# Optimization experiments

Measured on AMD Instinct MI355X. Metric: run time of the kernel, lower is better.

## Reference

```python
import jax, jax.numpy as jnp
import numpy as np

NUM_HEADS = 4
SPLIT = 2
DIM_FULL = 384  # constructor dim; scale uses dim // num_heads
SCALE = (DIM_FULL // NUM_HEADS) ** -0.5


def img2windows(img, ws, nh):
    # img: (B, D, H, W, C) -> (num_windows, nh, N, C//nh), N = prod(ws)
    B, D, H, W, C = img.shape
    d, h, w = ws
    x = img.reshape(B, D // d, d, H // h, h, W // w, w, C)
    x = x.transpose(0, 1, 3, 5, 2, 4, 6, 7).reshape(-1, d * h * w, C)
    return x.reshape(-1, d * h * w, nh, C // nh).transpose(0, 2, 1, 3)


def windows2img(xw, ws, B, D, H, W):
    # xw: (num_windows, d, h, w, C) -> (B, D, H, W, C)
    d, h, w = ws
    x = xw.reshape(B, D // d, H // h, W // w, d, h, w, -1)
    return x.transpose(0, 1, 4, 2, 5, 3, 6, 7).reshape(B, D, H, W, -1)


def setup_inputs() -> dict:
    key = jax.random.key(0)
    ks = jax.random.split(key, 5)
    B, D, H, W, C = 2, 8, 64, 64, 96
    qkv = jax.random.normal(ks[0], (3, B, D, H, W, C), jnp.float32)
    conv_w = jax.random.normal(ks[1], (C, 1, 3, 3, 3), jnp.float32) * 0.1  # depthwise Conv3d weight (O, I/groups, kD, kH, kW)
    conv_b = jax.random.normal(ks[2], (C,), jnp.float32) * 0.01
    proj_w = jax.random.normal(ks[3], (C, C), jnp.float32) * (C ** -0.5)  # torch Linear weight (out, in)
    proj_b = jax.random.normal(ks[4], (C,), jnp.float32) * 0.01
    return {"qkv": qkv, "conv_w": conv_w, "conv_b": conv_b, "proj_w": proj_w, "proj_b": proj_b}


def reference(qkv, conv_w, conv_b, proj_w, proj_b):
    q, k, v = qkv[0], qkv[1], qkv[2]
    B, D, H, W, C = q.shape
    ws = (1, H, SPLIT)  # idx == 0: (D_sp, H_sp, W_sp) = (1, H, split_size)
    qw = img2windows(q, ws, NUM_HEADS) * SCALE  # (nw, nh, N, hd)
    kw = img2windows(k, ws, NUM_HEADS)
    vw = img2windows(v, ws, NUM_HEADS)
    # LePE: depthwise 3x3x3 conv over v in NCDHW layout
    x = v.transpose(0, 4, 1, 2, 3)
    lepe = jax.lax.conv_general_dilated(
        x, conv_w, window_strides=(1, 1, 1), padding=[(1, 1)] * 3,
        dimension_numbers=("NCDHW", "OIDHW", "NCDHW"),
        feature_group_count=C) + conv_b[None, :, None, None, None]
    lepe = lepe.transpose(0, 2, 3, 4, 1)
    lepew = img2windows(lepe, ws, NUM_HEADS)
    # per-window attention
    attn = jax.nn.softmax(jnp.einsum("whnd,whmd->whnm", qw, kw), axis=-1)
    out = jnp.einsum("whnm,whmd->whnd", attn, vw) + lepew  # (nw, nh, N, hd)
    N = qw.shape[2]
    out = out.transpose(0, 2, 1, 3).reshape(-1, N, C)
    out = out @ proj_w.T + proj_b
    out = out.reshape(-1, ws[0], ws[1], ws[2], C)
    return windows2img(out, ws, B, D, H, W)
```

## Files before the change

### kernel.cpp

```cpp
#include <hip/hip_runtime.h>
#include <hip/hip_bf16.h>

constexpr int D_ = 8, H_ = 64, W_ = 64, C_ = 96;
constexpr int WC    = W_ * C_;
constexpr int HWC   = H_ * W_ * C_;
constexpr int BDHWC = 2 * D_ * HWC;
constexpr float SCALE = 0.10206207261596577f;

typedef __attribute__((ext_vector_type(4))) float f32x4;
typedef __attribute__((ext_vector_type(8))) short s16x8;

__device__ inline ushort f2bf(float x) {
  union { __hip_bfloat16 h; ushort u; } c;
  c.h = __float2bfloat16(x);
  return c.u;
}
__device__ inline float bf2f(ushort u) {
  union { float f; unsigned i; } c;
  c.i = ((unsigned)u) << 16;
  return c.f;
}
__device__ inline int xswz8(int bid, int nwg) {
  return (bid & 7) * (nwg >> 3) + (bid >> 3);
}

constexpr int QSTR  = 40;
constexpr int PSTR  = 136;
constexpr int PSTR2 = 72;

template <bool WSOUT>
__global__ void __launch_bounds__(256, 4)
attn_mfma_kernel(const float* __restrict__ qkv, float* __restrict__ out,
                 ushort* __restrict__ ws) {
  __shared__ ushort sK[128 * QSTR];
  __shared__ ushort sVt[32 * PSTR];
  __shared__ ushort sP[128 * PSTR2];

  const int t    = threadIdx.x;
  const int bid  = xswz8(blockIdx.x, 2048);
  const int head = bid & 3;
  const int nw   = bid >> 2;
  const int wq   = nw & 31;
  const int d    = (nw >> 5) & 7;
  const int b    = nw >> 8;
  const int hc   = head * 24;

  const float* qpl = qkv + (size_t)(b * 8 + d) * HWC;
  const float* kpl = qpl + BDHWC;
  const float* vpl = kpl + BDHWC;
  ushort* wvpl = ws + BDHWC + (size_t)(b * 8 + d) * HWC;

  {
    const s16x8 Z = {0, 0, 0, 0, 0, 0, 0, 0};
    int row = t >> 1, col = 24 + (t & 1) * 8;
    *reinterpret_cast<s16x8*>(&sK[row * QSTR + col]) = Z;
    if (t < 136) *reinterpret_cast<s16x8*>(&sVt[24 * PSTR + t * 8]) = Z;
  }

  #pragma unroll
  for (int it = 0; it < 3; ++it) {
    int idx = t + it * 256;
    int tok = idx / 6, c4 = (idx - tok * 6) * 4;
    int g = (tok >> 1) * WC + (wq * 2 + (tok & 1)) * 96 + hc + c4;
    float4 kv = *reinterpret_cast<const float4*>(kpl + g);
    float4 vv = *reinterpret_cast<const float4*>(vpl + g);
    ushort4 kh = { f2bf(kv.x), f2bf(kv.y), f2bf(kv.z), f2bf(kv.w) };
    ushort4 vh = { f2bf(vv.x), f2bf(vv.y), f2bf(vv.z), f2bf(vv.w) };
    *reinterpret_cast<ushort4*>(&sK[tok * QSTR + c4]) = kh;
    sVt[(c4 + 0) * PSTR + tok] = vh.x;
    sVt[(c4 + 1) * PSTR + tok] = vh.y;
    sVt[(c4 + 2) * PSTR + tok] = vh.z;
    sVt[(c4 + 3) * PSTR + tok] = vh.w;
    if (WSOUT) *reinterpret_cast<ushort4*>(wvpl + g) = vh;
  }

  const int wv = t >> 6, lane = t & 63;
  const int lr = lane & 15;
  const int lg = lane >> 4;
  const int r0 = (2 * wv) * 16;
  const int r1 = (2 * wv + 1) * 16;

  s16x8 a0 = {0,0,0,0,0,0,0,0}, a1 = {0,0,0,0,0,0,0,0};
  if (lg < 3) {
    union { s16x8 v; ushort u[8]; } qa;
    int tok = r0 + lr;
    const float* qp = qpl + (tok >> 1) * WC + (wq * 2 + (tok & 1)) * 96 + hc + lg * 8;
    float4 x0 = *reinterpret_cast<const float4*>(qp);
    float4 x1 = *reinterpret_cast<const float4*>(qp + 4);
    qa.u[0] = f2bf(x0.x * SCALE); qa.u[1] = f2bf(x0.y * SCALE);
    qa.u[2] = f2bf(x0.z * SCALE); qa.u[3] = f2bf(x0.w * SCALE);
    qa.u[4] = f2bf(x1.x * SCALE); qa.u[5] = f2bf(x1.y * SCALE);
    qa.u[6] = f2bf(x1.z * SCALE); qa.u[7] = f2bf(x1.w * SCALE);
    a0 = qa.v;
    tok = r1 + lr;
    qp = qpl + (tok >> 1) * WC + (wq * 2 + (tok & 1)) * 96 + hc + lg * 8;
    x0 = *reinterpret_cast<const float4*>(qp);
    x1 = *reinterpret_cast<const float4*>(qp + 4);
    qa.u[0] = f2bf(x0.x * SCALE); qa.u[1] = f2bf(x0.y * SCALE);
    qa.u[2] = f2bf(x0.z * SCALE); qa.u[3] = f2bf(x0.w * SCALE);
    qa.u[4] = f2bf(x1.x * SCALE); qa.u[5] = f2bf(x1.y * SCALE);
    qa.u[6] = f2bf(x1.z * SCALE); qa.u[7] = f2bf(x1.w * SCALE);
    a1 = qa.v;
  }

  __syncthreads();

  float rsum[2][4];
  #pragma unroll
  for (int rb = 0; rb < 2; ++rb)
    #pragma unroll
    for (int r = 0; r < 4; ++r) rsum[rb][r] = 0.f;

  f32x4 accO[2][2];
  #pragma unroll
  for (int i = 0; i < 2; ++i)
    #pragma unroll
    for (int j = 0; j < 2; ++j) accO[i][j] = f32x4{0.f, 0.f, 0.f, 0.f};

  #pragma unroll
  for (int half = 0; half < 2; ++half) {
    f32x4 accS[2][4];
    #pragma unroll
    for (int i = 0; i < 2; ++i)
      #pragma unroll
      for (int j = 0; j < 4; ++j) accS[i][j] = f32x4{0.f, 0.f, 0.f, 0.f};

    #pragma unroll
    for (int nb = 0; nb < 4; ++nb) {
      s16x8 bb = *reinterpret_cast<const s16x8*>(
          &sK[(half * 64 + nb * 16 + lr) * QSTR + lg * 8]);
      accS[0][nb] = __builtin_amdgcn_mfma_f32_16x16x32_bf16(a0, bb, accS[0][nb], 0, 0, 0);
      accS[1][nb] = __builtin_amdgcn_mfma_f32_16x16x32_bf16(a1, bb, accS[1][nb], 0, 0, 0);
    }

    #pragma unroll
    for (int rb = 0; rb < 2; ++rb)
      #pragma unroll
      for (int nb = 0; nb < 4; ++nb)
        #pragma unroll
        for (int r = 0; r < 4; ++r) {
          float e = __expf(accS[rb][nb][r]);
          accS[rb][nb][r] = e;
          rsum[rb][r] += e;
        }

    if (half) __syncthreads();

    #pragma unroll
    for (int rb = 0; rb < 2; ++rb)
      #pragma unroll
      for (int nb = 0; nb < 4; ++nb)
        #pragma unroll
        for (int r = 0; r < 4; ++r)
          sP[((2 * wv + rb) * 16 + lg * 4 + r) * PSTR2 + nb * 16 + lr] =
              f2bf(accS[rb][nb][r]);
    __syncthreads();

    #pragma unroll
    for (int kb = 0; kb < 2; ++kb) {
      int kc = half * 64 + kb * 32 + lg * 8;
      s16x8 pa0 = *reinterpret_cast<const s16x8*>(&sP[(r0 + lr) * PSTR2 + kb * 32 + lg * 8]);
      s16x8 pa1 = *reinterpret_cast<const s16x8*>(&sP[(r1 + lr) * PSTR2 + kb * 32 + lg * 8]);
      s16x8 vb0 = *reinterpret_cast<const s16x8*>(&sVt[lr * PSTR + kc]);
      s16x8 vb1 = *reinterpret_cast<const s16x8*>(&sVt[(16 + lr) * PSTR + kc]);
      accO[0][0] = __builtin_amdgcn_mfma_f32_16x16x32_bf16(pa0, vb0, accO[0][0], 0, 0, 0);
      accO[0][1] = __builtin_amdgcn_mfma_f32_16x16x32_bf16(pa0, vb1, accO[0][1], 0, 0, 0);
      accO[1][0] = __builtin_amdgcn_mfma_f32_16x16x32_bf16(pa1, vb0, accO[1][0], 0, 0, 0);
      accO[1][1] = __builtin_amdgcn_mfma_f32_16x16x32_bf16(pa1, vb1, accO[1][1], 0, 0, 0);
    }
  }

  float* opl   = out + (size_t)(b * 8 + d) * HWC;
  ushort* wpl  = ws  + (size_t)(b * 8 + d) * HWC;
  #pragma unroll
  for (int rb = 0; rb < 2; ++rb) {
    #pragma unroll
    for (int r = 0; r < 4; ++r) {
      float s = rsum[rb][r];
      s += __shfl_xor(s, 1); s += __shfl_xor(s, 2);
      s += __shfl_xor(s, 4); s += __shfl_xor(s, 8);
      int tok = (2 * wv + rb) * 16 + lg * 4 + r;
      int g = (tok >> 1) * WC + (wq * 2 + (tok & 1)) * 96 + hc;
      float inv = 1.0f / s;
      if (WSOUT) {
        wpl[g + lr] = f2bf(accO[rb][0][r] * inv);
        if (lr < 8) wpl[g + 16 + lr] = f2bf(accO[rb][1][r] * inv);
      } else {
        opl[g + lr] = accO[rb][0][r] * inv;
        if (lr < 8) opl[g + 16 + lr] = accO[rb][1][r] * inv;
      }
    }
  }
}

constexpr int VSTR = 104;
constexpr int WSTR = 104;

template <bool WSIN>
__global__ void __launch_bounds__(256, 4)
lepe_proj_fused_kernel(const float* __restrict__ qkv, const float* __restrict__ cw,
                       const float* __restrict__ cbias, const float* __restrict__ pw,
                       const float* __restrict__ pb, float* __restrict__ io,
                       const ushort* __restrict__ ws) {
  __shared__ ushort sV[66 * VSTR];
  __shared__ ushort sW[96 * WSTR];
  __shared__ ushort sCW[27 * 96];
  __shared__ float  sCB[96];
  __shared__ float  sPB[96];

  const int t   = threadIdx.x;
  const int bid = xswz8(blockIdx.x, 1024);
  const int h   = bid & 63;
  const int d   = (bid >> 6) & 7;
  const int b   = bid >> 9;

  float* iop = io + (size_t)(b * 8 + d) * HWC + h * WC;
  const ushort* wsp = ws + (size_t)(b * 8 + d) * HWC + h * WC;
  const ushort* wvb = ws + BDHWC + (size_t)b * 8 * HWC;
  const float* vbatch = qkv + 2 * (size_t)BDHWC + (size_t)b * 8 * HWC;

  const int tt  = t >> 2;
  const int cbk = (t & 3) * 24;

  float lep[24];
  if (WSIN) {
    union { s16x8 v; ushort u[8]; } azu[3];
    #pragma unroll
    for (int k = 0; k < 3; ++k)
      azu[k].v = *reinterpret_cast<const s16x8*>(wsp + tt * 96 + cbk + k * 8);
    #pragma unroll
    for (int k = 0; k < 3; ++k)
      #pragma unroll
      for (int e = 0; e < 8; ++e) lep[8*k+e] = bf2f(azu[k].u[e]);
  } else {
    float4 az[6];
    #pragma unroll
    for (int j = 0; j < 6; ++j)
      az[j] = *reinterpret_cast<const float4*>(iop + tt * 96 + cbk + j * 4);
    #pragma unroll
    for (int j = 0; j < 6; ++j) {
      lep[4*j+0] = az[j].x; lep[4*j+1] = az[j].y;
      lep[4*j+2] = az[j].z; lep[4*j+3] = az[j].w;
    }
  }

  if (t < 26) {
    const s16x8 Z = {0, 0, 0, 0, 0, 0, 0, 0};
    int row = (t < 13) ? 0 : 65;
    int col = (t < 13 ? t : t - 13) * 8;
    *reinterpret_cast<s16x8*>(&sV[row * VSTR + col]) = Z;
  }

  #pragma unroll
  for (int it = 0; it < 9; ++it) {
    int idx = t + it * 256;
    int co = idx / 24, c4 = (idx - co * 24) * 4;
    float4 x = *reinterpret_cast<const float4*>(pw + co * 96 + c4);
    ushort4 hx = { f2bf(x.x), f2bf(x.y), f2bf(x.z), f2bf(x.w) };
    *reinterpret_cast<ushort4*>(&sW[co * WSTR + c4]) = hx;
  }
  for (int idx = t; idx < 2592; idx += 256) {
    int c = idx / 27, tap = idx - c * 27;
    sCW[tap * 96 + c] = f2bf(cw[idx]);
  }
  if (t < 96) { sCB[t] = cbias[t]; sPB[t] = pb[t]; }

  #define TAP(row, tap)                                                      \
    {                                                                        \
      _Pragma("unroll")                                                      \
      for (int j8 = 0; j8 < 3; ++j8) {                                       \
        union { s16x8 v; ushort u[8]; } vu;                                  \
        vu.v = *reinterpret_cast<const s16x8*>(&sV[(row) * VSTR + cbk + j8 * 8]); \
        union { s16x8 v; ushort u[8]; } wu;                                  \
        wu.v = *reinterpret_cast<const s16x8*>(&sCW[(tap) * 96 + cbk + j8 * 8]); \
        _Pragma("unroll")                                                    \
        for (int e = 0; e < 8; ++e)                                          \
          lep[8*j8+e] = fmaf(bf2f(vu.u[e]), bf2f(wu.u[e]), lep[8*j8+e]);     \
      }                                                                      \
    }

  #pragma unroll
  for (int dd = 0; dd < 3; ++dd) {
    int zd = d + dd - 1;
    if (zd < 0 || zd >= D_) continue;
    #pragma unroll
    for (int dh = 0; dh < 3; ++dh) {
      int zh = h + dh - 1;
      if (zh < 0 || zh >= H_) continue;
      __syncthreads();
      if (WSIN) {
        const ushort* vrow = wvb + (size_t)zd * HWC + zh * WC;
        #pragma unroll
        for (int it = 0; it < 3; ++it) {
          int idx = t + it * 256;
          int tok = idx / 12, c8 = idx - tok * 12;
          s16x8 x = *reinterpret_cast<const s16x8*>(vrow + tok * 96 + c8 * 8);
          *reinterpret_cast<s16x8*>(&sV[(tok + 1) * VSTR + c8 * 8]) = x;
        }
      } else {
        const float4* src = reinterpret_cast<const float4*>(
            vbatch + (size_t)zd * HWC + zh * WC);
        #pragma unroll
        for (int it = 0; it < 6; ++it) {
          int idx = t + it * 256;
          int tok = idx / 24, c4 = idx - tok * 24;
          float4 x = src[idx];
          ushort4 hx = { f2bf(x.x), f2bf(x.y), f2bf(x.z), f2bf(x.w) };
          *reinterpret_cast<ushort4*>(&sV[(tok + 1) * VSTR + c4 * 4]) = hx;
        }
      }
      __syncthreads();
      const int tap0 = dd * 9 + dh * 3;
      TAP(tt,     tap0 + 0);
      TAP(tt + 1, tap0 + 1);
      TAP(tt + 2, tap0 + 2);
    }
  }
  #undef TAP

  __syncthreads();
  #pragma unroll
  for (int j = 0; j < 6; ++j) {
    float4 bz = *reinterpret_cast<const float4*>(sCB + cbk + j * 4);
    ushort4 hx = { f2bf(lep[4*j+0] + bz.x), f2bf(lep[4*j+1] + bz.y),
                   f2bf(lep[4*j+2] + bz.z), f2bf(lep[4*j+3] + bz.w) };
    *reinterpret_cast<ushort4*>(&sV[tt * VSTR + cbk + j * 4]) = hx;
  }
  __syncthreads();

  const int wv = t >> 6, lane = t & 63;
  const int lr = lane & 15, lg = lane >> 4;

  f32x4 acc[6];
  #pragma unroll
  for (int cb = 0; cb < 6; ++cb) {
    float bv = sPB[cb * 16 + lr];
    acc[cb] = f32x4{bv, bv, bv, bv};
  }
  s16x8 afr[3];
  #pragma unroll
  for (int kb = 0; kb < 3; ++kb)
    afr[kb] = *reinterpret_cast<const s16x8*>(&sV[(wv * 16 + lr) * VSTR + kb * 32 + lg * 8]);
  #pragma unroll
  for (int kb = 0; kb < 3; ++kb) {
    #pragma unroll
    for (int cb = 0; cb < 6; ++cb) {
      s16x8 bfr = *reinterpret_cast<const s16x8*>(&sW[(cb * 16 + lr) * WSTR + kb * 32 + lg * 8]);
      acc[cb] = __builtin_amdgcn_mfma_f32_16x16x32_bf16(afr[kb], bfr, acc[cb], 0, 0, 0);
    }
  }

  #pragma unroll
  for (int cb = 0; cb < 6; ++cb) {
    #pragma unroll
    for (int r = 0; r < 4; ++r) {
      int tok = wv * 16 + lg * 4 + r;
      iop[tok * 96 + cb * 16 + lr] = acc[cb][r];
    }
  }
}

extern "C" void kernel_launch(void* const* d_in, const int* in_sizes, int n_in,
                              void* d_out, int out_size, void* d_ws, size_t ws_size,
                              hipStream_t stream) {
  const float* qkv = (const float*)d_in[0];
  const float* cw  = (const float*)d_in[1];
  const float* cb  = (const float*)d_in[2];
  const float* pw  = (const float*)d_in[3];
  const float* pb  = (const float*)d_in[4];
  float* out = (float*)d_out;
  ushort* ws = (ushort*)d_ws;

  const size_t need = (size_t)2 * BDHWC * sizeof(ushort);
  if (ws_size >= need) {
    hipLaunchKernelGGL((attn_mfma_kernel<true>), dim3(2048), dim3(256), 0, stream,
                       qkv, out, ws);
    hipLaunchKernelGGL((lepe_proj_fused_kernel<true>), dim3(1024), dim3(256), 0, stream,
                       qkv, cw, cb, pw, pb, out, ws);
  } else {
    hipLaunchKernelGGL((attn_mfma_kernel<false>), dim3(2048), dim3(256), 0, stream,
                       qkv, out, ws);
    hipLaunchKernelGGL((lepe_proj_fused_kernel<false>), dim3(1024), dim3(256), 0, stream,
                       qkv, cw, cb, pw, pb, out, ws);
  }
}
```

Measured before the change: 56.66 us.

## Stage three H-rows of V per depth slice to cut barriers in LePE conv

The depthwise conv loop now loads all three neighbouring H rows for a given depth offset into three separate shared-memory buffers, with one barrier pair per depth slice instead of per (depth, height) pair. Out-of-range rows are zero-filled so the tap loop runs unconditionally. This cuts barriers and lets the row loads overlap, but it triples the sV footprint and lowers the launch-bounds occupancy hint from 4 to 2 blocks.

```diff
diff --git a/kernel.cpp b/kernel.cpp
--- a/kernel.cpp
+++ b/kernel.cpp
@@ -197,12 +197,12 @@
 constexpr int WSTR = 104;
 
 template <bool WSIN>
-__global__ void __launch_bounds__(256, 4)
+__global__ void __launch_bounds__(256, 2)
 lepe_proj_fused_kernel(const float* __restrict__ qkv, const float* __restrict__ cw,
                        const float* __restrict__ cbias, const float* __restrict__ pw,
                        const float* __restrict__ pb, float* __restrict__ io,
                        const ushort* __restrict__ ws) {
-  __shared__ ushort sV[66 * VSTR];
+  __shared__ ushort sV[3][66 * VSTR];
   __shared__ ushort sW[96 * WSTR];
   __shared__ ushort sCW[27 * 96];
   __shared__ float  sCB[96];
@@ -244,11 +244,12 @@
     }
   }
 
-  if (t < 26) {
+  if (t < 78) {
     const s16x8 Z = {0, 0, 0, 0, 0, 0, 0, 0};
-    int row = (t < 13) ? 0 : 65;
-    int col = (t < 13 ? t : t - 13) * 8;
-    *reinterpret_cast<s16x8*>(&sV[row * VSTR + col]) = Z;
+    int buf = t / 26, rr = t - buf * 26;
+    int row = (rr < 13) ? 0 : 65;
+    int col = (rr < 13 ? rr : rr - 13) * 8;
+    *reinterpret_cast<s16x8*>(&sV[buf][row * VSTR + col]) = Z;
   }
 
   #pragma unroll
@@ -265,12 +266,12 @@
   }
   if (t < 96) { sCB[t] = cbias[t]; sPB[t] = pb[t]; }
 
-  #define TAP(row, tap)                                                      \
+  #define TAP(BUF, row, tap)                                                 \
     {                                                                        \
       _Pragma("unroll")                                                      \
       for (int j8 = 0; j8 < 3; ++j8) {                                       \
         union { s16x8 v; ushort u[8]; } vu;                                  \
-        vu.v = *reinterpret_cast<const s16x8*>(&sV[(row) * VSTR + cbk + j8 * 8]); \
+        vu.v = *reinterpret_cast<const s16x8*>(&sV[BUF][(row) * VSTR + cbk + j8 * 8]); \
         union { s16x8 v; ushort u[8]; } wu;                                  \
         wu.v = *reinterpret_cast<const s16x8*>(&sCW[(tap) * 96 + cbk + j8 * 8]); \
         _Pragma("unroll")                                                    \
@@ -283,37 +284,51 @@
   for (int dd = 0; dd < 3; ++dd) {
     int zd = d + dd - 1;
     if (zd < 0 || zd >= D_) continue;
+    __syncthreads();
+
     #pragma unroll
     for (int dh = 0; dh < 3; ++dh) {
       int zh = h + dh - 1;
-      if (zh < 0 || zh >= H_) continue;
-      __syncthreads();
-      if (WSIN) {
-        const ushort* vrow = wvb + (size_t)zd * HWC + zh * WC;
+      if (zh >= 0 && zh < H_) {
+        if (WSIN) {
+          const ushort* vrow = wvb + (size_t)zd * HWC + zh * WC;
+          #pragma unroll
+          for (int it = 0; it < 3; ++it) {
+            int idx = t + it * 256;
+            int tok = idx / 12, c8 = idx - tok * 12;
+            s16x8 x = *reinterpret_cast<const s16x8*>(vrow + tok * 96 + c8 * 8);
+            *reinterpret_cast<s16x8*>(&sV[dh][(tok + 1) * VSTR + c8 * 8]) = x;
+          }
+        } else {
+          const float4* src = reinterpret_cast<const float4*>(
+              vbatch + (size_t)zd * HWC + zh * WC);
+          #pragma unroll
+          for (int it = 0; it < 6; ++it) {
+            int idx = t + it * 256;
+            int tok = idx / 24, c4 = idx - tok * 24;
+            float4 x = src[idx];
+            ushort4 hx = { f2bf(x.x), f2bf(x.y), f2bf(x.z), f2bf(x.w) };
+            *reinterpret_cast<ushort4*>(&sV[dh][(tok + 1) * VSTR + c4 * 4]) = hx;
+          }
+        }
+      } else {
+        const s16x8 Z = {0, 0, 0, 0, 0, 0, 0, 0};
         #pragma unroll
         for (int it = 0; it < 3; ++it) {
           int idx = t + it * 256;
           int tok = idx / 12, c8 = idx - tok * 12;
-          s16x8 x = *reinterpret_cast<const s16x8*>(vrow + tok * 96 + c8 * 8);
-          *reinterpret_cast<s16x8*>(&sV[(tok + 1) * VSTR + c8 * 8]) = x;
-        }
-      } else {
-        const float4* src = reinterpret_cast<const float4*>(
-            vbatch + (size_t)zd * HWC + zh * WC);
-        #pragma unroll
-        for (int it = 0; it < 6; ++it) {
-          int idx = t + it * 256;
-          int tok = idx / 24, c4 = idx - tok * 24;
-          float4 x = src[idx];
-          ushort4 hx = { f2bf(x.x), f2bf(x.y), f2bf(x.z), f2bf(x.w) };
-          *reinterpret_cast<ushort4*>(&sV[(tok + 1) * VSTR + c4 * 4]) = hx;
+          *reinterpret_cast<s16x8*>(&sV[dh][(tok + 1) * VSTR + c8 * 8]) = Z;
         }
       }
-      __syncthreads();
-      const int tap0 = dd * 9 + dh * 3;
-      TAP(tt,     tap0 + 0);
-      TAP(tt + 1, tap0 + 1);
-      TAP(tt + 2, tap0 + 2);
+    }
+    __syncthreads();
+
+    const int tap0 = dd * 9;
+    #pragma unroll
+    for (int dh = 0; dh < 3; ++dh) {
+      TAP(dh, tt,     tap0 + dh * 3 + 0);
+      TAP(dh, tt + 1, tap0 + dh * 3 + 1);
+      TAP(dh, tt + 2, tap0 + dh * 3 + 2);
     }
   }
   #undef TAP
@@ -324,7 +339,7 @@
     float4 bz = *reinterpret_cast<const float4*>(sCB + cbk + j * 4);
     ushort4 hx = { f2bf(lep[4*j+0] + bz.x), f2bf(lep[4*j+1] + bz.y),
                    f2bf(lep[4*j+2] + bz.z), f2bf(lep[4*j+3] + bz.w) };
-    *reinterpret_cast<ushort4*>(&sV[tt * VSTR + cbk + j * 4]) = hx;
+    *reinterpret_cast<ushort4*>(&sV[0][tt * VSTR + cbk + j * 4]) = hx;
   }
   __syncthreads();
 
@@ -340,7 +355,7 @@
   s16x8 afr[3];
   #pragma unroll
   for (int kb = 0; kb < 3; ++kb)
-    afr[kb] = *reinterpret_cast<const s16x8*>(&sV[(wv * 16 + lr) * VSTR + kb * 32 + lg * 8]);
+    afr[kb] = *reinterpret_cast<const s16x8*>(&sV[0][(wv * 16 + lr) * VSTR + kb * 32 + lg * 8]);
   #pragma unroll
   for (int kb = 0; kb < 3; ++kb) {
     #pragma unroll
```

Result: slower. 62.11 us (+9.6%).

## Double-buffer LePE row loads with async global-to-LDS DMA in fused proj kernel

Applied to the files above, without the earlier changes.

Reworks the depthwise-conv row staging in the fused LePE+projection kernel to use two LDS buffers filled by global_load_lds, so the next (d,h) row is prefetched while the current one is convolved. This cuts the sync/load latency between taps. Padded halo rows are replaced by clamped indices and multiplicative edge masks, and out-of-range rows are still loaded but skipped, which keeps control flow uniform. Launch bounds drop from 4 to 2 waves per EU to fit the larger LDS footprint, which may reduce occupancy.

```diff
diff --git a/kernel.cpp b/kernel.cpp
--- a/kernel.cpp
+++ b/kernel.cpp
@@ -193,16 +193,15 @@
   }
 }
 
-constexpr int VSTR = 104;
 constexpr int WSTR = 104;
 
 template <bool WSIN>
-__global__ void __launch_bounds__(256, 4)
+__global__ void __launch_bounds__(256, 2)
 lepe_proj_fused_kernel(const float* __restrict__ qkv, const float* __restrict__ cw,
                        const float* __restrict__ cbias, const float* __restrict__ pw,
                        const float* __restrict__ pb, float* __restrict__ io,
                        const ushort* __restrict__ ws) {
-  __shared__ ushort sV[66 * VSTR];
+  __shared__ ushort sV2[2][64 * 96];
   __shared__ ushort sW[96 * WSTR];
   __shared__ ushort sCW[27 * 96];
   __shared__ float  sCB[96];
@@ -214,6 +213,8 @@
   const int d   = (bid >> 6) & 7;
   const int b   = bid >> 9;
 
+  const int wvq = t >> 6, lane = t & 63;
+
   float* iop = io + (size_t)(b * 8 + d) * HWC + h * WC;
   const ushort* wsp = ws + (size_t)(b * 8 + d) * HWC + h * WC;
   const ushort* wvb = ws + BDHWC + (size_t)b * 8 * HWC;
@@ -242,13 +243,6 @@
       lep[4*j+0] = az[j].x; lep[4*j+1] = az[j].y;
       lep[4*j+2] = az[j].z; lep[4*j+3] = az[j].w;
     }
-  }
-
-  if (t < 26) {
-    const s16x8 Z = {0, 0, 0, 0, 0, 0, 0, 0};
-    int row = (t < 13) ? 0 : 65;
-    int col = (t < 13 ? t : t - 13) * 8;
-    *reinterpret_cast<s16x8*>(&sV[row * VSTR + col]) = Z;
   }
 
   #pragma unroll
@@ -265,12 +259,28 @@
   }
   if (t < 96) { sCB[t] = cbias[t]; sPB[t] = pb[t]; }
 
-  #define TAP(row, tap)                                                      \
+  int   zdc[3], zhc[3];
+  float fdc[3], fhc[3];
+  #pragma unroll
+  for (int j = 0; j < 3; ++j) {
+    int zd = d + j - 1;
+    fdc[j] = (zd >= 0 && zd < D_) ? 1.f : 0.f;
+    zdc[j] = zd < 0 ? 0 : (zd > D_ - 1 ? D_ - 1 : zd);
+    int zh = h + j - 1;
+    fhc[j] = (zh >= 0 && zh < H_) ? 1.f : 0.f;
+    zhc[j] = zh < 0 ? 0 : (zh > H_ - 1 ? H_ - 1 : zh);
+  }
+  const float fwl0 = (tt > 0)  ? 1.f : 0.f;
+  const float fwl2 = (tt < 63) ? 1.f : 0.f;
+  const int   zw0  = (tt > 0)  ? tt - 1 : 0;
+  const int   zw2  = (tt < 63) ? tt + 1 : 63;
+
+  #define TAPC(BI, row, tap)                                                 \
     {                                                                        \
       _Pragma("unroll")                                                      \
       for (int j8 = 0; j8 < 3; ++j8) {                                       \
         union { s16x8 v; ushort u[8]; } vu;                                  \
-        vu.v = *reinterpret_cast<const s16x8*>(&sV[(row) * VSTR + cbk + j8 * 8]); \
+        vu.v = *reinterpret_cast<const s16x8*>(&sV2[BI][(row) * 96 + cbk + j8 * 8]); \
         union { s16x8 v; ushort u[8]; } wu;                                  \
         wu.v = *reinterpret_cast<const s16x8*>(&sCW[(tap) * 96 + cbk + j8 * 8]); \
         _Pragma("unroll")                                                    \
@@ -278,26 +288,59 @@
           lep[8*j8+e] = fmaf(bf2f(vu.u[e]), bf2f(wu.u[e]), lep[8*j8+e]);     \
       }                                                                      \
     }
-
-  #pragma unroll
-  for (int dd = 0; dd < 3; ++dd) {
-    int zd = d + dd - 1;
-    if (zd < 0 || zd >= D_) continue;
-    #pragma unroll
-    for (int dh = 0; dh < 3; ++dh) {
-      int zh = h + dh - 1;
-      if (zh < 0 || zh >= H_) continue;
+  #define TAPE(BI, row, tap, FW)                                             \
+    {                                                                        \
+      _Pragma("unroll")                                                      \
+      for (int j8 = 0; j8 < 3; ++j8) {                                       \
+        union { s16x8 v; ushort u[8]; } vu;                                  \
+        vu.v = *reinterpret_cast<const s16x8*>(&sV2[BI][(row) * 96 + cbk + j8 * 8]); \
+        union { s16x8 v; ushort u[8]; } wu;                                  \
+        wu.v = *reinterpret_cast<const s16x8*>(&sCW[(tap) * 96 + cbk + j8 * 8]); \
+        _Pragma("unroll")                                                    \
+        for (int e = 0; e < 8; ++e)                                          \
+          lep[8*j8+e] = fmaf(bf2f(vu.u[e]) * (FW), bf2f(wu.u[e]), lep[8*j8+e]); \
+      }                                                                      \
+    }
+  #define DMA(zd, zh, BI)                                                    \
+    {                                                                        \
+      const ushort* vrow_ = wvb + (size_t)(zd) * HWC + (zh) * WC;            \
+      _Pragma("unroll")                                                      \
+      for (int c_ = 0; c_ < 3; ++c_) {                                       \
+        int ch_ = c_ * 4 + wvq;                                              \
+        __builtin_amdgcn_global_load_lds(                                    \
+            (const __attribute__((address_space(1))) void*)(vrow_ + ch_ * 512 + lane * 8), \
+            (__attribute__((address_space(3))) void*)(&sV2[BI][ch_ * 512]),  \
+            16, 0, 0);                                                       \
+      }                                                                      \
+    }
+
+  if (WSIN) {
+    DMA(zdc[0], zhc[0], 0);
+    __syncthreads();
+    #pragma unroll
+    for (int r = 0; r < 9; ++r) {
+      const int dd = r / 3, dh = r - 3 * dd;
+      if (r < 8) {
+        const int nr = r + 1, nd = nr / 3, nh = nr - 3 * nd;
+        DMA(zdc[nd], zhc[nh], nr & 1);
+      }
+      if (fdc[dd] * fhc[dh] != 0.f) {
+        TAPE(r & 1, zw0, r * 3 + 0, fwl0);
+        TAPC(r & 1, tt,  r * 3 + 1);
+        TAPE(r & 1, zw2, r * 3 + 2, fwl2);
+      }
       __syncthreads();
-      if (WSIN) {
-        const ushort* vrow = wvb + (size_t)zd * HWC + zh * WC;
-        #pragma unroll
-        for (int it = 0; it < 3; ++it) {
-          int idx = t + it * 256;
-          int tok = idx / 12, c8 = idx - tok * 12;
-          s16x8 x = *reinterpret_cast<const s16x8*>(vrow + tok * 96 + c8 * 8);
-          *reinterpret_cast<s16x8*>(&sV[(tok + 1) * VSTR + c8 * 8]) = x;
-        }
-      } else {
+    }
+  } else {
+    #pragma unroll
+    for (int dd = 0; dd < 3; ++dd) {
+      int zd = d + dd - 1;
+      if (zd < 0 || zd >= D_) continue;
+      #pragma unroll
+      for (int dh = 0; dh < 3; ++dh) {
+        int zh = h + dh - 1;
+        if (zh < 0 || zh >= H_) continue;
+        __syncthreads();
         const float4* src = reinterpret_cast<const float4*>(
             vbatch + (size_t)zd * HWC + zh * WC);
         #pragma unroll
@@ -306,29 +349,30 @@
           int tok = idx / 24, c4 = idx - tok * 24;
           float4 x = src[idx];
           ushort4 hx = { f2bf(x.x), f2bf(x.y), f2bf(x.z), f2bf(x.w) };
-          *reinterpret_cast<ushort4*>(&sV[(tok + 1) * VSTR + c4 * 4]) = hx;
+          *reinterpret_cast<ushort4*>(&sV2[0][tok * 96 + c4 * 4]) = hx;
         }
+        __syncthreads();
+        const int tap0 = dd * 9 + dh * 3;
+        TAPE(0, zw0, tap0 + 0, fwl0);
+        TAPC(0, tt,  tap0 + 1);
+        TAPE(0, zw2, tap0 + 2, fwl2);
       }
-      __syncthreads();
-      const int tap0 = dd * 9 + dh * 3;
-      TAP(tt,     tap0 + 0);
-      TAP(tt + 1, tap0 + 1);
-      TAP(tt + 2, tap0 + 2);
-    }
-  }
-  #undef TAP
-
-  __syncthreads();
+    }
+    __syncthreads();
+  }
+  #undef TAPC
+  #undef TAPE
+  #undef DMA
+
   #pragma unroll
   for (int j = 0; j < 6; ++j) {
     float4 bz = *reinterpret_cast<const float4*>(sCB + cbk + j * 4);
     ushort4 hx = { f2bf(lep[4*j+0] + bz.x), f2bf(lep[4*j+1] + bz.y),
                    f2bf(lep[4*j+2] + bz.z), f2bf(lep[4*j+3] + bz.w) };
-    *reinterpret_cast<ushort4*>(&sV[tt * VSTR + cbk + j * 4]) = hx;
+    *reinterpret_cast<ushort4*>(&sV2[0][tt * 96 + cbk + j * 4]) = hx;
   }
   __syncthreads();
 
-  const int wv = t >> 6, lane = t & 63;
   const int lr = lane & 15, lg = lane >> 4;
 
   f32x4 acc[6];
@@ -340,7 +384,7 @@
   s16x8 afr[3];
   #pragma unroll
   for (int kb = 0; kb < 3; ++kb)
-    afr[kb] = *reinterpret_cast<const s16x8*>(&sV[(wv * 16 + lr) * VSTR + kb * 32 + lg * 8]);
+    afr[kb] = *reinterpret_cast<const s16x8*>(&sV2[0][(wvq * 16 + lr) * 96 + kb * 32 + lg * 8]);
   #pragma unroll
   for (int kb = 0; kb < 3; ++kb) {
     #pragma unroll
@@ -354,7 +398,7 @@
   for (int cb = 0; cb < 6; ++cb) {
     #pragma unroll
     for (int r = 0; r < 4; ++r) {
-      int tok = wv * 16 + lg * 4 + r;
+      int tok = wvq * 16 + lg * 4 + r;
       iop[tok * 96 + cb * 16 + lr] = acc[cb][r];
     }
   }
```

After: 56.06 us. No clear change (-1.0%).
